# Performance work log

Hardware: AMD Instinct MI355X
Metric: run time of the kernel (lower is better)

The kernel has to match this reference:

```python
import jax, jax.numpy as jnp
import numpy as np

BN_EPS = 0.001

def conv2d(x, w, b, stride, pad):
    # x: NCHW, w: OIHW
    y = jax.lax.conv_general_dilated(x, w, (stride, stride), [(pad, pad), (pad, pad)],
                                     dimension_numbers=('NCHW', 'OIHW', 'NCHW'))
    return y + b[None, :, None, None]

def up2(x):
    return jnp.repeat(jnp.repeat(x, 2, axis=2), 2, axis=3)

def bn_eval(x, g, b):
    # BatchNorm in eval mode with fresh running stats (mean=0, var=1)
    inv = g / jnp.sqrt(1.0 + BN_EPS)
    return inv[None, :, None, None] * x + b[None, :, None, None]

def setup_inputs() -> dict:
    key = jax.random.key(0)
    ks = jax.random.split(key, 16)
    inp = {}
    inp['x_init'] = jax.random.uniform(ks[0], (8, 3, 1024, 1024), dtype=jnp.float32)
    inp['thresh'] = jax.random.uniform(ks[1], (2,), dtype=jnp.float32)
    inp['sample_w'] = jax.random.normal(ks[2], (3, 3, 4, 4), dtype=jnp.float32) * 0.1
    inp['sample_b'] = jax.random.normal(ks[3], (3,), dtype=jnp.float32) * 0.1
    inp['centers'] = jax.random.uniform(ks[4], (8,), dtype=jnp.float32)
    inp['pool1_w'] = jax.random.normal(ks[5], (3, 3, 2, 2), dtype=jnp.float32) * 0.2
    inp['pool1_b'] = jax.random.normal(ks[6], (3,), dtype=jnp.float32) * 0.1
    inp['pool2_w'] = jax.random.normal(ks[7], (3, 3, 2, 2), dtype=jnp.float32) * 0.2
    inp['pool2_b'] = jax.random.normal(ks[8], (3,), dtype=jnp.float32) * 0.1
    inp['ctx_conv_w'] = jax.random.normal(ks[9], (4, 3, 3, 3, 3), dtype=jnp.float32) * 0.2
    inp['ctx_conv_b'] = jax.random.normal(ks[10], (4, 3), dtype=jnp.float32) * 0.1
    inp['ctx_bn_g'] = jax.random.uniform(ks[11], (4, 3), dtype=jnp.float32) + 0.5
    inp['ctx_bn_b'] = jax.random.normal(ks[12], (4, 3), dtype=jnp.float32) * 0.1
    return inp

def _quant_idx_counts(t, mask, centers):
    # counts[k] = #(elements of t with mask and argmin center == k)
    idx = jnp.argmin((t[..., None] - centers) ** 2, axis=-1)  # same shape as t
    oh = idx[..., None] == jnp.arange(centers.shape[0])
    return jnp.sum((mask[..., None] & oh).astype(jnp.float32), axis=(0, 1, 2, 3))

def reference(x_init, thresh, sample_w, sample_b, centers,
              pool1_w, pool1_b, pool2_w, pool2_b,
              ctx_conv_w, ctx_conv_b, ctx_bn_g, ctx_bn_b):
    # spectral norm of sample conv weight (exact largest singular value)
    sigma = jnp.linalg.svd(sample_w.reshape(sample_w.shape[0], -1), compute_uv=False)[0]
    x = conv2d(x_init, sample_w / sigma, sample_b, 4, 0)  # [B,3,H/4,W/4]
    B, C, H, W = x.shape

    # ContextExtractor: conv_i(relu(bn_i(h))), stride 2 each
    h = x_init
    for i in range(3):
        h = conv2d(jax.nn.relu(bn_eval(h, ctx_bn_g[i], ctx_bn_b[i])), ctx_conv_w[i], ctx_conv_b[i], 2, 1)
    h1 = conv2d(jax.nn.relu(bn_eval(h, ctx_bn_g[3], ctx_bn_b[3])), ctx_conv_w[3], ctx_conv_b[3], 2, 1)
    feat_1 = (jnp.tanh(h) + 1.0) / 2.0    # [B,3,H/8,W/8]
    feat_2 = (jnp.tanh(h1) + 1.0) / 2.0   # [B,3,H/16,W/16]

    th_1, th_2 = thresh[0], thresh[1]
    feat_1_ = up2(feat_1)
    feat_2_ = up2(up2(feat_2))

    p1 = conv2d(x, pool1_w, pool1_b, 2, 0)    # half res
    p2 = conv2d(p1, pool2_w, pool2_b, 2, 0)   # quarter res
    ss_1 = up2(p1)
    ss_2 = up2(up2(p2))

    cond_2 = feat_2_ < th_2
    cond_1 = jnp.logical_and(jnp.logical_not(cond_2), feat_1_ < th_1)
    cond_0 = jnp.logical_not(jnp.logical_or(cond_1, cond_2))
    mask_1 = jnp.logical_and(up2(feat_2) >= th_2, feat_1 < th_1)  # half-res mask for p1
    mask_2 = feat_2 < th_2                                         # quarter-res mask for p2

    xq = jnp.where(cond_1, ss_1, x)
    xq = jnp.where(cond_2, ss_2, xq)

    # soft vector quantization against 8 learned centers
    d = (xq[..., None] - centers) ** 2                 # [B,C,H,W,8]
    soft = jnp.sum(centers * jax.nn.softmax(-d, axis=-1), axis=-1)

    # compression statistics (esti_cr; huffman real_cr omitted - host-side, non-tensor)
    esti_size = (jnp.sum(cond_0.astype(jnp.float32))
                 + jnp.sum(cond_1.astype(jnp.float32)) / 4.0
                 + jnp.sum(cond_2.astype(jnp.float32)) / 16.0)
    esti_cr = (1.0 / 16.0) * esti_size / (H * W * C * B)

    # histogram std over comp_data quantization indices, via masked counts
    counts = (_quant_idx_counts(x, cond_0, centers)
              + _quant_idx_counts(p1, mask_1, centers)
              + _quant_idx_counts(p2, mask_2, centers))
    counts = counts / jnp.sum(counts)
    std = jnp.std(counts, ddof=1)

    return (soft, esti_cr, std)
```

## Files before the change

kernel.cpp:

```cpp
#include <hip/hip_runtime.h>
#include <math.h>


#define SENT -1e30f
#define BSTR 72
#define BCH  (17 * BSTR)

__device__ __forceinline__ float featf(float h) { return 0.5f * (tanhf(h) + 1.0f); }

__device__ __forceinline__ void stage_raw(const float* __restrict__ base,
                                          float* __restrict__ L,
                                          int gr0, int gc0, int S, int t) {
    #pragma unroll
    for (int p = 0; p < 2; p++) {
        int idx = t + 256 * p;
        if (idx < 289) {
            int lr = idx / 17;
            int s  = idx - lr * 17;
            int gr = gr0 + lr;
            int gc = gc0 - 4 + 4 * s;
            float4 v;
            if (gr >= 0 && gr < S && gc >= 0)
                v = *(const float4*)(base + (size_t)gr * S + gc);
            else { v.x = SENT; v.y = SENT; v.z = SENT; v.w = SENT; }
            *(float4*)&L[lr * BSTR + 4 * s] = v;
        }
    }
}

__device__ __forceinline__ void stage_bn(const float* __restrict__ base,
                                         float* __restrict__ L,
                                         int gr0, int gc0, int S, int t,
                                         float inv, float bb) {
    #pragma unroll
    for (int p = 0; p < 2; p++) {
        int idx = t + 256 * p;
        if (idx < 289) {
            int lr = idx / 17;
            int s  = idx - lr * 17;
            int gr = gr0 + lr;
            int gc = gc0 - 4 + 4 * s;
            float4 v;
            if (gr >= 0 && gr < S && gc >= 0)
                v = *(const float4*)(base + (size_t)gr * S + gc);
            else { v.x = SENT; v.y = SENT; v.z = SENT; v.w = SENT; }
            v.x = fmaxf(fmaf(inv, v.x, bb), 0.0f);
            v.y = fmaxf(fmaf(inv, v.y, bb), 0.0f);
            v.z = fmaxf(fmaf(inv, v.z, bb), 0.0f);
            v.w = fmaxf(fmaf(inv, v.w, bb), 0.0f);
            *(float4*)&L[lr * BSTR + 4 * s] = v;
        }
    }
}

__global__ __launch_bounds__(256) void k_band_l0(
    const float* __restrict__ xin,
    const float* __restrict__ sw_g, const float* __restrict__ sb,
    const float* __restrict__ ctxw, const float* __restrict__ ctxb,
    const float* __restrict__ bng, const float* __restrict__ bnb,
    const float* __restrict__ p1w, const float* __restrict__ p1b,
    const float* __restrict__ p2w, const float* __restrict__ p2b,
    float* __restrict__ outX, float* __restrict__ outH0,
    float* __restrict__ outP1, float* __restrict__ outP2)
{
    __shared__ float sx[3 * BCH];

    int t = threadIdx.x, bid = blockIdx.x;
    int tileX = bid & 15, bandY = (bid >> 4) & 63, b = bid >> 10;

    int gr0 = bandY * 16 - 1;
    int gc0 = tileX * 64;
    #pragma unroll
    for (int c = 0; c < 3; c++)
        stage_raw(xin + ((size_t)(b * 3 + c) << 20), &sx[c * BCH], gr0, gc0, 1024, t);
    __syncthreads();

    {
        int ox = t & 31, oy = t >> 5;
        float v[3][9];
        const float* Lb = sx + (2 * oy) * BSTR + 2 * ox + 2;
        #pragma unroll
        for (int c = 0; c < 3; c++) {
            const float* Lc = Lb + c * BCH;
            #pragma unroll
            for (int kh = 0; kh < 3; kh++) {
                float2 u  = *(const float2*)(Lc + kh * BSTR);
                float2 w2 = *(const float2*)(Lc + kh * BSTR + 2);
                v[c][kh * 3 + 0] = u.y;
                v[c][kh * 3 + 1] = w2.x;
                v[c][kh * 3 + 2] = w2.y;
            }
        }
        #pragma unroll
        for (int c = 0; c < 3; c++) {
            float inv = bng[c] / sqrtf(1.001f), bb = bnb[c];
            #pragma unroll
            for (int k = 0; k < 9; k++)
                v[c][k] = fmaxf(fmaf(inv, v[c][k], bb), 0.0f);
        }
        float a0 = ctxb[0], a1 = ctxb[1], a2 = ctxb[2];
        #pragma unroll
        for (int c = 0; c < 3; c++)
            #pragma unroll
            for (int k = 0; k < 9; k++) {
                float tv = v[c][k];
                a0 = fmaf(ctxw[c * 9 + k],      tv, a0);
                a1 = fmaf(ctxw[27 + c * 9 + k], tv, a1);
                a2 = fmaf(ctxw[54 + c * 9 + k], tv, a2);
            }
        unsigned o = (unsigned)(b * 3) * 262144u
                   + (unsigned)(bandY * 8 + oy) * 512u + tileX * 32 + ox;
        outH0[o] = a0; outH0[o + 262144u] = a1; outH0[o + 524288u] = a2;
    }

    if (t < 64) {
        float p00 = 0.f, p01 = 0.f, p02 = 0.f, p11 = 0.f, p12 = 0.f, p22 = 0.f;
        if (t < 48) {
            float a0 = sw_g[t], a1 = sw_g[48 + t], a2 = sw_g[96 + t];
            p00 = a0 * a0; p01 = a0 * a1; p02 = a0 * a2;
            p11 = a1 * a1; p12 = a1 * a2; p22 = a2 * a2;
        }
        #pragma unroll
        for (int off = 32; off > 0; off >>= 1) {
            p00 += __shfl_down(p00, off); p01 += __shfl_down(p01, off);
            p02 += __shfl_down(p02, off); p11 += __shfl_down(p11, off);
            p12 += __shfl_down(p12, off); p22 += __shfl_down(p22, off);
        }
        float inv_sigma = 0.0f;
        if (t == 0) {
            float q = (p00 + p11 + p22) * (1.0f / 3.0f);
            float pp1 = p01 * p01 + p02 * p02 + p12 * p12;
            float pp2 = (p00 - q) * (p00 - q) + (p11 - q) * (p11 - q)
                      + (p22 - q) * (p22 - q) + 2.0f * pp1;
            float lam;
            if (pp2 < 1e-30f) lam = q;
            else {
                float pr = sqrtf(pp2 / 6.0f);
                float B00 = (p00 - q) / pr, B01 = p01 / pr, B02 = p02 / pr;
                float B11 = (p11 - q) / pr, B12 = p12 / pr, B22 = (p22 - q) / pr;
                float detB = B00 * (B11 * B22 - B12 * B12)
                           - B01 * (B01 * B22 - B12 * B02)
                           + B02 * (B01 * B12 - B11 * B02);
                float r = fminf(1.0f, fmaxf(-1.0f, 0.5f * detB));
                lam = q + 2.0f * pr * cosf(acosf(r) * (1.0f / 3.0f));
            }
            double G00 = p00, G01 = p01, G02 = p02, G11 = p11, G12 = p12, G22 = p22;
            double c2 = G00 + G11 + G22;
            double c1 = G00 * G11 - G01 * G01 + G00 * G22 - G02 * G02 + G11 * G22 - G12 * G12;
            double c0 = G00 * (G11 * G22 - G12 * G12) - G01 * (G01 * G22 - G12 * G02)
                      + G02 * (G01 * G12 - G11 * G02);
            double L = (double)lam;
            #pragma unroll
            for (int it = 0; it < 2; it++) {
                double pv = ((L - c2) * L + c1) * L - c0;
                double dv = (3.0 * L - 2.0 * c2) * L + c1;
                L -= pv / dv;
            }
            inv_sigma = (float)(1.0 / sqrt(L));
        }
        inv_sigma = __shfl(inv_sigma, 0);

        int xl = t & 15, yl = t >> 4;
        float4 r[3][4];
        #pragma unroll
        for (int c = 0; c < 3; c++)
            #pragma unroll
            for (int kh = 0; kh < 4; kh++)
                r[c][kh] = *(const float4*)&sx[c * BCH + (4 * yl + kh + 1) * BSTR + 4 * xl + 4];
        float s0 = 0.f, s1 = 0.f, s2 = 0.f;
        #pragma unroll
        for (int c = 0; c < 3; c++)
            #pragma unroll
            for (int kh = 0; kh < 4; kh++) {
                float4 vv = r[c][kh];
                const float* w0 = &sw_g[(0 * 3 + c) * 16 + kh * 4];
                const float* w1 = &sw_g[(1 * 3 + c) * 16 + kh * 4];
                const float* w2 = &sw_g[(2 * 3 + c) * 16 + kh * 4];
                s0 += w0[0] * vv.x + w0[1] * vv.y + w0[2] * vv.z + w0[3] * vv.w;
                s1 += w1[0] * vv.x + w1[1] * vv.y + w1[2] * vv.z + w1[3] * vv.w;
                s2 += w2[0] * vv.x + w2[1] * vv.y + w2[2] * vv.z + w2[3] * vv.w;
            }
        float x0 = fmaf(s0, inv_sigma, sb[0]);
        float x1 = fmaf(s1, inv_sigma, sb[1]);
        float x2 = fmaf(s2, inv_sigma, sb[2]);
        unsigned o = (unsigned)(b * 3) * 65536u
                   + (unsigned)(bandY * 4 + yl) * 256u + tileX * 16 + xl;
        outX[o] = x0; outX[o + 65536u] = x1; outX[o + 131072u] = x2;

        int sl = 2 * (t & 7) + 16 * (2 * ((t >> 3) & 1));
        float q0 = p1b[0], q1 = p1b[1], q2 = p1b[2];
        #pragma unroll
        for (int dy = 0; dy < 2; dy++)
            #pragma unroll
            for (int dx = 0; dx < 2; dx++) {
                int src = sl + dx + 16 * dy;
                float vx0 = __shfl(x0, src);
                float vx1 = __shfl(x1, src);
                float vx2 = __shfl(x2, src);
                int wi = dy * 2 + dx;
                q0 = fmaf(p1w[wi], vx0, q0); q0 = fmaf(p1w[4 + wi],  vx1, q0); q0 = fmaf(p1w[8 + wi],  vx2, q0);
                q1 = fmaf(p1w[12 + wi], vx0, q1); q1 = fmaf(p1w[16 + wi], vx1, q1); q1 = fmaf(p1w[20 + wi], vx2, q1);
                q2 = fmaf(p1w[24 + wi], vx0, q2); q2 = fmaf(p1w[28 + wi], vx1, q2); q2 = fmaf(p1w[32 + wi], vx2, q2);
            }
        if (t < 16) {
            int px = t & 7, py = t >> 3;
            unsigned op = (unsigned)(b * 3) * 16384u
                        + (unsigned)(bandY * 2 + py) * 128u + tileX * 8 + px;
            outP1[op] = q0; outP1[op + 16384u] = q1; outP1[op + 32768u] = q2;
        }

        int s2l = 2 * (t & 3);
        float r0 = p2b[0], r1 = p2b[1], r2 = p2b[2];
        #pragma unroll
        for (int dy = 0; dy < 2; dy++)
            #pragma unroll
            for (int dx = 0; dx < 2; dx++) {
                int src = s2l + dx + 8 * dy;
                float vq0 = __shfl(q0, src);
                float vq1 = __shfl(q1, src);
                float vq2 = __shfl(q2, src);
                int wi = dy * 2 + dx;
                r0 = fmaf(p2w[wi], vq0, r0); r0 = fmaf(p2w[4 + wi],  vq1, r0); r0 = fmaf(p2w[8 + wi],  vq2, r0);
                r1 = fmaf(p2w[12 + wi], vq0, r1); r1 = fmaf(p2w[16 + wi], vq1, r1); r1 = fmaf(p2w[20 + wi], vq2, r1);
                r2 = fmaf(p2w[24 + wi], vq0, r2); r2 = fmaf(p2w[28 + wi], vq1, r2); r2 = fmaf(p2w[32 + wi], vq2, r2);
            }
        if (t < 4) {
            unsigned op = (unsigned)(b * 3) * 4096u + (unsigned)bandY * 64u + tileX * 4 + t;
            outP2[op] = r0; outP2[op + 4096u] = r1; outP2[op + 8192u] = r2;
        }
    }
}

__global__ __launch_bounds__(256) void k_band_ctx(
    const float* __restrict__ in, float* __restrict__ outH, float* __restrict__ outF,
    const float* __restrict__ w, const float* __restrict__ bias,
    const float* __restrict__ bng, const float* __restrict__ bnb,
    int S, int tpxbits, int bandbits)
{
    __shared__ float sx[3 * BCH];
    int t = threadIdx.x, bid = blockIdx.x;
    int tileX = bid & ((1 << tpxbits) - 1);
    int bandY = (bid >> tpxbits) & ((1 << bandbits) - 1);
    int b = bid >> (tpxbits + bandbits);

    int gr0 = bandY * 16 - 1;
    int gc0 = tileX * 64;
    #pragma unroll
    for (int c = 0; c < 3; c++) {
        float inv = bng[c] / sqrtf(1.001f), bb = bnb[c];
        stage_bn(in + (size_t)(b * 3 + c) * S * S, &sx[c * BCH], gr0, gc0, S, t, inv, bb);
    }
    __syncthreads();

    int So = S >> 1;
    unsigned os = (unsigned)So * So;
    int ox = t & 31, oy = t >> 5;
    float v[3][9];
    const float* Lb = sx + (2 * oy) * BSTR + 2 * ox + 2;
    #pragma unroll
    for (int c = 0; c < 3; c++) {
        const float* Lc = Lb + c * BCH;
        #pragma unroll
        for (int kh = 0; kh < 3; kh++) {
            float2 u  = *(const float2*)(Lc + kh * BSTR);
            float2 w2 = *(const float2*)(Lc + kh * BSTR + 2);
            v[c][kh * 3 + 0] = u.y;
            v[c][kh * 3 + 1] = w2.x;
            v[c][kh * 3 + 2] = w2.y;
        }
    }
    float a0 = bias[0], a1 = bias[1], a2 = bias[2];
    #pragma unroll
    for (int c = 0; c < 3; c++)
        #pragma unroll
        for (int k = 0; k < 9; k++) {
            float tv = v[c][k];
            a0 = fmaf(w[c * 9 + k],      tv, a0);
            a1 = fmaf(w[27 + c * 9 + k], tv, a1);
            a2 = fmaf(w[54 + c * 9 + k], tv, a2);
        }
    unsigned o = (unsigned)(b * 3) * os + (unsigned)(bandY * 8 + oy) * So + tileX * 32 + ox;
    if (outH) { outH[o] = a0; outH[o + os] = a1; outH[o + 2 * os] = a2; }
    if (outF) { outF[o] = featf(a0); outF[o + os] = featf(a1); outF[o + 2 * os] = featf(a2); }
}

__device__ __forceinline__ int argmin8(float v, const float* __restrict__ sc) {
    float best = 1e30f; int ki = 0;
    #pragma unroll
    for (int k = 0; k < 8; k++) {
        float df = v - sc[k]; float dk = df * df;
        if (dk < best) { best = dk; ki = k; }
    }
    return ki;
}

__global__ __launch_bounds__(256) void k_final(
    const float* __restrict__ x, const float* __restrict__ f1,
    const float* __restrict__ f2, const float* __restrict__ p1,
    const float* __restrict__ p2, const float* __restrict__ thresh,
    const float* __restrict__ centers, float* __restrict__ out,
    int* __restrict__ partials)
{
    __shared__ int sh[4 * 12];
    int t = threadIdx.x;
    int lane = t & 63;
    int* shW = &sh[12 * (t >> 6)];
    if (lane < 12) shW[lane] = 0;
    float sc[8];
    #pragma unroll
    for (int k = 0; k < 8; k++) sc[k] = centers[k];
    __syncthreads();

    float th1 = thresh[0], th2 = thresh[1];
    int gid = blockIdx.x * 256 + t;
    int xc = gid & 255, y = (gid >> 8) & 255, b = gid >> 16;
    unsigned i2 = (unsigned)(((y >> 1) << 7) + (xc >> 1));
    unsigned i4 = (unsigned)(((y >> 2) << 6) + (xc >> 2));
    bool doM1 = ((y & 1) == 0) && ((xc & 1) == 0);
    bool doM2 = ((y & 3) == 0) && ((xc & 3) == 0);
    int c0n = 0, c1n = 0, c2n = 0;

    #pragma unroll
    for (int c = 0; c < 3; c++) {
        unsigned pc = (unsigned)(b * 3 + c);
        float f1v = f1[pc * 16384u + i2];
        float f2v = f2[pc * 4096u + i4];
        float p1v = p1[pc * 16384u + i2];
        float p2v = p2[pc * 4096u + i4];
        float xv  = x[pc * 65536u + (unsigned)((y << 8) + xc)];
        bool cond2 = f2v < th2;
        bool cond1 = (!cond2) && (f1v < th1);
        bool cond0 = !(cond1 || cond2);
        float xq = cond2 ? p2v : (cond1 ? p1v : xv);

        float d[8]; float dmin = 1e30f;
        #pragma unroll
        for (int k = 0; k < 8; k++) { float df = xq - sc[k]; d[k] = df * df; dmin = fminf(dmin, d[k]); }
        float se = 0.f, sn = 0.f;
        #pragma unroll
        for (int k = 0; k < 8; k++) { float e = __expf(dmin - d[k]); se += e; sn = fmaf(sc[k], e, sn); }
        out[pc * 65536u + (unsigned)((y << 8) + xc)] = sn / se;

        c0n += cond0; c1n += cond1; c2n += cond2;

        if (cond0) atomicAdd(&shW[argmin8(xv, sc)], 1);
        if (doM1 && (f2v >= th2) && (f1v < th1)) atomicAdd(&shW[argmin8(p1v, sc)], 1);
        if (doM2 && cond2) atomicAdd(&shW[argmin8(p2v, sc)], 1);
    }
    #pragma unroll
    for (int off = 32; off > 0; off >>= 1) {
        c0n += __shfl_down(c0n, off);
        c1n += __shfl_down(c1n, off);
        c2n += __shfl_down(c2n, off);
    }
    if (lane == 0) { atomicAdd(&shW[8], c0n); atomicAdd(&shW[9], c1n); atomicAdd(&shW[10], c2n); }
    __syncthreads();
    if (t < 12)
        partials[blockIdx.x * 12 + t] = sh[t] + sh[12 + t] + sh[24 + t] + sh[36 + t];
}

__global__ void k_reduce(const int* __restrict__ partials, float* __restrict__ out2) {
    __shared__ int accs[12];
    int t = threadIdx.x;
    if (t < 12) accs[t] = 0;
    __syncthreads();
    int s[12];
    #pragma unroll
    for (int k = 0; k < 12; k++) s[k] = 0;
    for (int r = t; r < 2048; r += 256) {
        const int* row = partials + r * 12;
        #pragma unroll
        for (int k = 0; k < 12; k++) s[k] += row[k];
    }
    #pragma unroll
    for (int k = 0; k < 12; k++) {
        #pragma unroll
        for (int off = 32; off > 0; off >>= 1) s[k] += __shfl_down(s[k], off);
    }
    if ((t & 63) == 0) {
        #pragma unroll
        for (int k = 0; k < 12; k++) if (s[k]) atomicAdd(&accs[k], s[k]);
    }
    __syncthreads();
    if (t == 0) {
        float cnt0 = (float)accs[8], cnt1 = (float)accs[9], cnt2 = (float)accs[10];
        float esti = cnt0 + cnt1 * 0.25f + cnt2 * 0.0625f;
        float cr = (1.0f / 16.0f) * esti / (256.0f * 256.0f * 3.0f * 8.0f);
        float cs[8]; float tot = 0.0f;
        #pragma unroll
        for (int k = 0; k < 8; k++) { cs[k] = (float)accs[k]; tot += cs[k]; }
        float mean = 0.0f;
        #pragma unroll
        for (int k = 0; k < 8; k++) { cs[k] /= tot; mean += cs[k]; }
        mean *= 0.125f;
        float var = 0.0f;
        #pragma unroll
        for (int k = 0; k < 8; k++) { float df = cs[k] - mean; var += df * df; }
        var *= (1.0f / 7.0f);
        out2[0] = cr;
        out2[1] = sqrtf(var);
    }
}

extern "C" void kernel_launch(void* const* d_in, const int* in_sizes, int n_in,
                              void* d_out, int out_size, void* d_ws, size_t ws_size,
                              hipStream_t stream) {
    const float* x_init   = (const float*)d_in[0];
    const float* thresh   = (const float*)d_in[1];
    const float* sample_w = (const float*)d_in[2];
    const float* sample_b = (const float*)d_in[3];
    const float* centers  = (const float*)d_in[4];
    const float* pool1_w  = (const float*)d_in[5];
    const float* pool1_b  = (const float*)d_in[6];
    const float* pool2_w  = (const float*)d_in[7];
    const float* pool2_b  = (const float*)d_in[8];
    const float* ctx_w    = (const float*)d_in[9];
    const float* ctx_b    = (const float*)d_in[10];
    const float* bn_g     = (const float*)d_in[11];
    const float* bn_b     = (const float*)d_in[12];
    float* out = (float*)d_out;

    float* wsf      = (float*)d_ws;
    int*   partials = (int*)wsf;
    float* bufX     = wsf + 32768;
    float* bufH0    = bufX  + 1572864;
    float* bufH1    = bufH0 + 6291456;
    float* bufH2    = bufH1 + 1572864;
    float* bufP1    = bufH2 + 393216;
    float* bufP2    = bufP1 + 393216;
    float* bufF1    = bufP2 + 98304;
    float* bufF2    = bufF1 + 393216;

    k_band_l0<<<8192, 256, 0, stream>>>(x_init, sample_w, sample_b,
                                        ctx_w, ctx_b, bn_g, bn_b,
                                        pool1_w, pool1_b, pool2_w, pool2_b,
                                        bufX, bufH0, bufP1, bufP2);
    k_band_ctx<<<2048, 256, 0, stream>>>(bufH0, bufH1, nullptr,
                                         ctx_w + 81,  ctx_b + 3, bn_g + 3, bn_b + 3,
                                         512, 3, 5);
    k_band_ctx<<<512, 256, 0, stream>>>(bufH1, bufH2, bufF1,
                                        ctx_w + 162, ctx_b + 6, bn_g + 6, bn_b + 6,
                                        256, 2, 4);
    k_band_ctx<<<128, 256, 0, stream>>>(bufH2, nullptr, bufF2,
                                        ctx_w + 243, ctx_b + 9, bn_g + 9, bn_b + 9,
                                        128, 1, 3);
    k_final<<<2048, 256, 0, stream>>>(bufX, bufF1, bufF2, bufP1, bufP2,
                                      thresh, centers, out, partials);
    k_reduce<<<1, 256, 0, stream>>>(partials, out + 1572864);
}
```

Measured before the change: 223.2 us.

## Fuse pairs of strided context conv layers via shared-memory halo recompute

Merges context conv layers 0 and 1 into the first kernel and layers 2 and 3 into a second kernel. Each block stages a larger halo tile, computes the intermediate layer into shared memory, and then applies the next conv. This removes the large H0 and H2 global round trips and two kernel launches. In exchange it adds redundant halo computation and more shared memory per block, and only 64 threads do the second-layer work.

```diff
diff --git a/kernel.cpp b/kernel.cpp
--- a/kernel.cpp
+++ b/kernel.cpp
@@ -3,120 +3,121 @@
 
 
 #define SENT -1e30f
-#define BSTR 72
-#define BCH  (17 * BSTR)
+#define SXSTR 72
+#define SXCH  (19 * SXSTR)
+#define H0STR 36
+#define H0CH  (9 * H0STR)
 
 __device__ __forceinline__ float featf(float h) { return 0.5f * (tanhf(h) + 1.0f); }
 
-__device__ __forceinline__ void stage_raw(const float* __restrict__ base,
-                                          float* __restrict__ L,
-                                          int gr0, int gc0, int S, int t) {
+__device__ __forceinline__ void stage19(const float* __restrict__ base,
+                                        float* __restrict__ L,
+                                        int gr0, int gc0, int S, int t) {
     #pragma unroll
     for (int p = 0; p < 2; p++) {
         int idx = t + 256 * p;
-        if (idx < 289) {
+        if (idx < 323) {
             int lr = idx / 17;
             int s  = idx - lr * 17;
             int gr = gr0 + lr;
-            int gc = gc0 - 4 + 4 * s;
+            int gc = gc0 + 4 * s;
             float4 v;
-            if (gr >= 0 && gr < S && gc >= 0)
+            if (gr >= 0 && gr < S && gc >= 0 && gc < S)
                 v = *(const float4*)(base + (size_t)gr * S + gc);
             else { v.x = SENT; v.y = SENT; v.z = SENT; v.w = SENT; }
-            *(float4*)&L[lr * BSTR + 4 * s] = v;
-        }
-    }
-}
-
-__device__ __forceinline__ void stage_bn(const float* __restrict__ base,
-                                         float* __restrict__ L,
-                                         int gr0, int gc0, int S, int t,
-                                         float inv, float bb) {
-    #pragma unroll
-    for (int p = 0; p < 2; p++) {
-        int idx = t + 256 * p;
-        if (idx < 289) {
-            int lr = idx / 17;
-            int s  = idx - lr * 17;
-            int gr = gr0 + lr;
-            int gc = gc0 - 4 + 4 * s;
-            float4 v;
-            if (gr >= 0 && gr < S && gc >= 0)
-                v = *(const float4*)(base + (size_t)gr * S + gc);
-            else { v.x = SENT; v.y = SENT; v.z = SENT; v.w = SENT; }
-            v.x = fmaxf(fmaf(inv, v.x, bb), 0.0f);
-            v.y = fmaxf(fmaf(inv, v.y, bb), 0.0f);
-            v.z = fmaxf(fmaf(inv, v.z, bb), 0.0f);
-            v.w = fmaxf(fmaf(inv, v.w, bb), 0.0f);
-            *(float4*)&L[lr * BSTR + 4 * s] = v;
-        }
-    }
-}
-
-__global__ __launch_bounds__(256) void k_band_l0(
+            *(float4*)&L[lr * SXSTR + 4 * s] = v;
+        }
+    }
+}
+
+__global__ __launch_bounds__(256) void k_fused01(
     const float* __restrict__ xin,
     const float* __restrict__ sw_g, const float* __restrict__ sb,
     const float* __restrict__ ctxw, const float* __restrict__ ctxb,
     const float* __restrict__ bng, const float* __restrict__ bnb,
     const float* __restrict__ p1w, const float* __restrict__ p1b,
     const float* __restrict__ p2w, const float* __restrict__ p2b,
-    float* __restrict__ outX, float* __restrict__ outH0,
+    float* __restrict__ outX, float* __restrict__ outH1,
     float* __restrict__ outP1, float* __restrict__ outP2)
 {
-    __shared__ float sx[3 * BCH];
+    __shared__ float sx[3 * SXCH];
+    __shared__ float sm[3 * H0CH];
 
     int t = threadIdx.x, bid = blockIdx.x;
     int tileX = bid & 15, bandY = (bid >> 4) & 63, b = bid >> 10;
 
-    int gr0 = bandY * 16 - 1;
-    int gc0 = tileX * 64;
+    int gr0 = bandY * 16 - 3;
+    int gc0 = tileX * 64 - 4;
     #pragma unroll
     for (int c = 0; c < 3; c++)
-        stage_raw(xin + ((size_t)(b * 3 + c) << 20), &sx[c * BCH], gr0, gc0, 1024, t);
+        stage19(xin + ((size_t)(b * 3 + c) << 20), &sx[c * SXCH], gr0, gc0, 1024, t);
     __syncthreads();
 
     {
-        int ox = t & 31, oy = t >> 5;
-        float v[3][9];
-        const float* Lb = sx + (2 * oy) * BSTR + 2 * ox + 2;
+        float inv0[3], bb0[3];
+        #pragma unroll
+        for (int c = 0; c < 3; c++) { inv0[c] = bng[c] / sqrtf(1.001f); bb0[c] = bnb[c]; }
+        #pragma unroll
+        for (int p = 0; p < 2; p++) {
+            int idx = t + 256 * p;
+            if (idx < 297) {
+                int lhy = idx / 33;
+                int lhx = idx - 33 * lhy;
+                bool oob = (bandY == 0 && lhy == 0) || (tileX == 0 && lhx == 0);
+                float a0 = ctxb[0], a1 = ctxb[1], a2 = ctxb[2];
+                #pragma unroll
+                for (int c = 0; c < 3; c++) {
+                    const float* basep = &sx[c * SXCH + 2 * lhy * SXSTR + 2 * lhx];
+                    float inv = inv0[c], bb = bb0[c];
+                    #pragma unroll
+                    for (int kh = 0; kh < 3; kh++) {
+                        float2 c0 = *(const float2*)(basep + kh * SXSTR);
+                        float2 c1 = *(const float2*)(basep + kh * SXSTR + 2);
+                        float t0 = fmaxf(fmaf(inv, c0.y, bb), 0.0f);
+                        float t1 = fmaxf(fmaf(inv, c1.x, bb), 0.0f);
+                        float t2 = fmaxf(fmaf(inv, c1.y, bb), 0.0f);
+                        int wi = c * 9 + kh * 3;
+                        a0 = fmaf(ctxw[wi], t0, a0); a0 = fmaf(ctxw[wi + 1], t1, a0); a0 = fmaf(ctxw[wi + 2], t2, a0);
+                        a1 = fmaf(ctxw[27 + wi], t0, a1); a1 = fmaf(ctxw[28 + wi], t1, a1); a1 = fmaf(ctxw[29 + wi], t2, a1);
+                        a2 = fmaf(ctxw[54 + wi], t0, a2); a2 = fmaf(ctxw[55 + wi], t1, a2); a2 = fmaf(ctxw[56 + wi], t2, a2);
+                    }
+                }
+                int o = lhy * H0STR + lhx;
+                if (oob) { a0 = SENT; a1 = SENT; a2 = SENT; }
+                sm[o] = a0; sm[H0CH + o] = a1; sm[2 * H0CH + o] = a2;
+            }
+        }
+    }
+    __syncthreads();
+
+    if (t < 64) {
+        int lx = t & 15, ly = t >> 4;
+        const float* w1c = ctxw + 81;
+        float a0 = ctxb[3], a1 = ctxb[4], a2 = ctxb[5];
         #pragma unroll
         for (int c = 0; c < 3; c++) {
-            const float* Lc = Lb + c * BCH;
+            float inv = bng[3 + c] / sqrtf(1.001f), bb = bnb[3 + c];
+            const float* mb = &sm[c * H0CH + 2 * ly * H0STR + 2 * lx];
             #pragma unroll
             for (int kh = 0; kh < 3; kh++) {
-                float2 u  = *(const float2*)(Lc + kh * BSTR);
-                float2 w2 = *(const float2*)(Lc + kh * BSTR + 2);
-                v[c][kh * 3 + 0] = u.y;
-                v[c][kh * 3 + 1] = w2.x;
-                v[c][kh * 3 + 2] = w2.y;
-            }
-        }
-        #pragma unroll
-        for (int c = 0; c < 3; c++) {
-            float inv = bng[c] / sqrtf(1.001f), bb = bnb[c];
-            #pragma unroll
-            for (int k = 0; k < 9; k++)
-                v[c][k] = fmaxf(fmaf(inv, v[c][k], bb), 0.0f);
-        }
-        float a0 = ctxb[0], a1 = ctxb[1], a2 = ctxb[2];
-        #pragma unroll
-        for (int c = 0; c < 3; c++)
-            #pragma unroll
-            for (int k = 0; k < 9; k++) {
-                float tv = v[c][k];
-                a0 = fmaf(ctxw[c * 9 + k],      tv, a0);
-                a1 = fmaf(ctxw[27 + c * 9 + k], tv, a1);
-                a2 = fmaf(ctxw[54 + c * 9 + k], tv, a2);
-            }
-        unsigned o = (unsigned)(b * 3) * 262144u
-                   + (unsigned)(bandY * 8 + oy) * 512u + tileX * 32 + ox;
-        outH0[o] = a0; outH0[o + 262144u] = a1; outH0[o + 524288u] = a2;
-    }
-
-    if (t < 64) {
+                float2 c0 = *(const float2*)(mb + kh * H0STR);
+                float c2v = mb[kh * H0STR + 2];
+                float t0 = fmaxf(fmaf(inv, c0.x, bb), 0.0f);
+                float t1 = fmaxf(fmaf(inv, c0.y, bb), 0.0f);
+                float t2 = fmaxf(fmaf(inv, c2v, bb), 0.0f);
+                int wi = c * 9 + kh * 3;
+                a0 = fmaf(w1c[wi], t0, a0); a0 = fmaf(w1c[wi + 1], t1, a0); a0 = fmaf(w1c[wi + 2], t2, a0);
+                a1 = fmaf(w1c[27 + wi], t0, a1); a1 = fmaf(w1c[28 + wi], t1, a1); a1 = fmaf(w1c[29 + wi], t2, a1);
+                a2 = fmaf(w1c[54 + wi], t0, a2); a2 = fmaf(w1c[55 + wi], t1, a2); a2 = fmaf(w1c[56 + wi], t2, a2);
+            }
+        }
+        unsigned o = (unsigned)(b * 3) * 65536u + (unsigned)(bandY * 4 + ly) * 256u + tileX * 16 + lx;
+        outH1[o] = a0; outH1[o + 65536u] = a1; outH1[o + 131072u] = a2;
+    } else if (t < 128) {
+        int tl = t - 64;
         float p00 = 0.f, p01 = 0.f, p02 = 0.f, p11 = 0.f, p12 = 0.f, p22 = 0.f;
-        if (t < 48) {
-            float a0 = sw_g[t], a1 = sw_g[48 + t], a2 = sw_g[96 + t];
+        if (tl < 48) {
+            float a0 = sw_g[tl], a1 = sw_g[48 + tl], a2 = sw_g[96 + tl];
             p00 = a0 * a0; p01 = a0 * a1; p02 = a0 * a2;
             p11 = a1 * a1; p12 = a1 * a2; p22 = a2 * a2;
         }
@@ -127,7 +128,7 @@
             p12 += __shfl_down(p12, off); p22 += __shfl_down(p22, off);
         }
         float inv_sigma = 0.0f;
-        if (t == 0) {
+        if (tl == 0) {
             float q = (p00 + p11 + p22) * (1.0f / 3.0f);
             float pp1 = p01 * p01 + p02 * p02 + p12 * p12;
             float pp2 = (p00 - q) * (p00 - q) + (p11 - q) * (p11 - q)
@@ -160,13 +161,13 @@
         }
         inv_sigma = __shfl(inv_sigma, 0);
 
-        int xl = t & 15, yl = t >> 4;
+        int xl = tl & 15, yl = tl >> 4;
         float4 r[3][4];
         #pragma unroll
         for (int c = 0; c < 3; c++)
             #pragma unroll
             for (int kh = 0; kh < 4; kh++)
-                r[c][kh] = *(const float4*)&sx[c * BCH + (4 * yl + kh + 1) * BSTR + 4 * xl + 4];
+                r[c][kh] = *(const float4*)&sx[c * SXCH + (4 * yl + 3 + kh) * SXSTR + 4 * xl + 4];
         float s0 = 0.f, s1 = 0.f, s2 = 0.f;
         #pragma unroll
         for (int c = 0; c < 3; c++)
@@ -183,11 +184,10 @@
         float x0 = fmaf(s0, inv_sigma, sb[0]);
         float x1 = fmaf(s1, inv_sigma, sb[1]);
         float x2 = fmaf(s2, inv_sigma, sb[2]);
-        unsigned o = (unsigned)(b * 3) * 65536u
-                   + (unsigned)(bandY * 4 + yl) * 256u + tileX * 16 + xl;
+        unsigned o = (unsigned)(b * 3) * 65536u + (unsigned)(bandY * 4 + yl) * 256u + tileX * 16 + xl;
         outX[o] = x0; outX[o + 65536u] = x1; outX[o + 131072u] = x2;
 
-        int sl = 2 * (t & 7) + 16 * (2 * ((t >> 3) & 1));
+        int sl = 2 * (tl & 7) + 32 * ((tl >> 3) & 1);
         float q0 = p1b[0], q1 = p1b[1], q2 = p1b[2];
         #pragma unroll
         for (int dy = 0; dy < 2; dy++)
@@ -202,14 +202,13 @@
                 q1 = fmaf(p1w[12 + wi], vx0, q1); q1 = fmaf(p1w[16 + wi], vx1, q1); q1 = fmaf(p1w[20 + wi], vx2, q1);
                 q2 = fmaf(p1w[24 + wi], vx0, q2); q2 = fmaf(p1w[28 + wi], vx1, q2); q2 = fmaf(p1w[32 + wi], vx2, q2);
             }
-        if (t < 16) {
-            int px = t & 7, py = t >> 3;
-            unsigned op = (unsigned)(b * 3) * 16384u
-                        + (unsigned)(bandY * 2 + py) * 128u + tileX * 8 + px;
+        if (tl < 16) {
+            int px = tl & 7, py = tl >> 3;
+            unsigned op = (unsigned)(b * 3) * 16384u + (unsigned)(bandY * 2 + py) * 128u + tileX * 8 + px;
             outP1[op] = q0; outP1[op + 16384u] = q1; outP1[op + 32768u] = q2;
         }
 
-        int s2l = 2 * (t & 3);
+        int s2l = 2 * (tl & 3);
         float r0 = p2b[0], r1 = p2b[1], r2 = p2b[2];
         #pragma unroll
         for (int dy = 0; dy < 2; dy++)
@@ -224,64 +223,98 @@
                 r1 = fmaf(p2w[12 + wi], vq0, r1); r1 = fmaf(p2w[16 + wi], vq1, r1); r1 = fmaf(p2w[20 + wi], vq2, r1);
                 r2 = fmaf(p2w[24 + wi], vq0, r2); r2 = fmaf(p2w[28 + wi], vq1, r2); r2 = fmaf(p2w[32 + wi], vq2, r2);
             }
-        if (t < 4) {
-            unsigned op = (unsigned)(b * 3) * 4096u + (unsigned)bandY * 64u + tileX * 4 + t;
+        if (tl < 4) {
+            unsigned op = (unsigned)(b * 3) * 4096u + (unsigned)bandY * 64u + tileX * 4 + tl;
             outP2[op] = r0; outP2[op + 4096u] = r1; outP2[op + 8192u] = r2;
         }
     }
 }
 
-__global__ __launch_bounds__(256) void k_band_ctx(
-    const float* __restrict__ in, float* __restrict__ outH, float* __restrict__ outF,
-    const float* __restrict__ w, const float* __restrict__ bias,
-    const float* __restrict__ bng, const float* __restrict__ bnb,
-    int S, int tpxbits, int bandbits)
+__global__ __launch_bounds__(256) void k_fused23(
+    const float* __restrict__ h1, float* __restrict__ outF1, float* __restrict__ outF2,
+    const float* __restrict__ ctxw, const float* __restrict__ ctxb,
+    const float* __restrict__ bng, const float* __restrict__ bnb)
 {
-    __shared__ float sx[3 * BCH];
+    __shared__ float sx[3 * SXCH];
+    __shared__ float sm[3 * H0CH];
+
     int t = threadIdx.x, bid = blockIdx.x;
-    int tileX = bid & ((1 << tpxbits) - 1);
-    int bandY = (bid >> tpxbits) & ((1 << bandbits) - 1);
-    int b = bid >> (tpxbits + bandbits);
-
-    int gr0 = bandY * 16 - 1;
-    int gc0 = tileX * 64;
-    #pragma unroll
-    for (int c = 0; c < 3; c++) {
-        float inv = bng[c] / sqrtf(1.001f), bb = bnb[c];
-        stage_bn(in + (size_t)(b * 3 + c) * S * S, &sx[c * BCH], gr0, gc0, S, t, inv, bb);
-    }
-    __syncthreads();
-
-    int So = S >> 1;
-    unsigned os = (unsigned)So * So;
-    int ox = t & 31, oy = t >> 5;
-    float v[3][9];
-    const float* Lb = sx + (2 * oy) * BSTR + 2 * ox + 2;
-    #pragma unroll
-    for (int c = 0; c < 3; c++) {
-        const float* Lc = Lb + c * BCH;
-        #pragma unroll
-        for (int kh = 0; kh < 3; kh++) {
-            float2 u  = *(const float2*)(Lc + kh * BSTR);
-            float2 w2 = *(const float2*)(Lc + kh * BSTR + 2);
-            v[c][kh * 3 + 0] = u.y;
-            v[c][kh * 3 + 1] = w2.x;
-            v[c][kh * 3 + 2] = w2.y;
-        }
-    }
-    float a0 = bias[0], a1 = bias[1], a2 = bias[2];
+    int tileX = bid & 3, bandY = (bid >> 2) & 15, b = bid >> 6;
+
+    int gr0 = bandY * 16 - 3;
+    int gc0 = tileX * 64 - 4;
     #pragma unroll
     for (int c = 0; c < 3; c++)
-        #pragma unroll
-        for (int k = 0; k < 9; k++) {
-            float tv = v[c][k];
-            a0 = fmaf(w[c * 9 + k],      tv, a0);
-            a1 = fmaf(w[27 + c * 9 + k], tv, a1);
-            a2 = fmaf(w[54 + c * 9 + k], tv, a2);
-        }
-    unsigned o = (unsigned)(b * 3) * os + (unsigned)(bandY * 8 + oy) * So + tileX * 32 + ox;
-    if (outH) { outH[o] = a0; outH[o + os] = a1; outH[o + 2 * os] = a2; }
-    if (outF) { outF[o] = featf(a0); outF[o + os] = featf(a1); outF[o + 2 * os] = featf(a2); }
+        stage19(h1 + (size_t)(b * 3 + c) * 65536, &sx[c * SXCH], gr0, gc0, 256, t);
+    __syncthreads();
+
+    {
+        const float* w2c = ctxw + 162;
+        float inv2[3], bb2[3];
+        #pragma unroll
+        for (int c = 0; c < 3; c++) { inv2[c] = bng[6 + c] / sqrtf(1.001f); bb2[c] = bnb[6 + c]; }
+        #pragma unroll
+        for (int p = 0; p < 2; p++) {
+            int idx = t + 256 * p;
+            if (idx < 297) {
+                int lhy = idx / 33;
+                int lhx = idx - 33 * lhy;
+                bool oob = (bandY == 0 && lhy == 0) || (tileX == 0 && lhx == 0);
+                float a0 = ctxb[6], a1 = ctxb[7], a2 = ctxb[8];
+                #pragma unroll
+                for (int c = 0; c < 3; c++) {
+                    const float* basep = &sx[c * SXCH + 2 * lhy * SXSTR + 2 * lhx];
+                    float inv = inv2[c], bb = bb2[c];
+                    #pragma unroll
+                    for (int kh = 0; kh < 3; kh++) {
+                        float2 c0 = *(const float2*)(basep + kh * SXSTR);
+                        float2 c1 = *(const float2*)(basep + kh * SXSTR + 2);
+                        float t0 = fmaxf(fmaf(inv, c0.y, bb), 0.0f);
+                        float t1 = fmaxf(fmaf(inv, c1.x, bb), 0.0f);
+                        float t2 = fmaxf(fmaf(inv, c1.y, bb), 0.0f);
+                        int wi = c * 9 + kh * 3;
+                        a0 = fmaf(w2c[wi], t0, a0); a0 = fmaf(w2c[wi + 1], t1, a0); a0 = fmaf(w2c[wi + 2], t2, a0);
+                        a1 = fmaf(w2c[27 + wi], t0, a1); a1 = fmaf(w2c[28 + wi], t1, a1); a1 = fmaf(w2c[29 + wi], t2, a1);
+                        a2 = fmaf(w2c[54 + wi], t0, a2); a2 = fmaf(w2c[55 + wi], t1, a2); a2 = fmaf(w2c[56 + wi], t2, a2);
+                    }
+                }
+                int o = lhy * H0STR + lhx;
+                if (!oob && lhy >= 1 && lhx >= 1) {
+                    unsigned fo = (unsigned)(b * 3) * 16384u
+                                + (unsigned)(8 * bandY + lhy - 1) * 128u + 32 * tileX + lhx - 1;
+                    outF1[fo] = featf(a0); outF1[fo + 16384u] = featf(a1); outF1[fo + 32768u] = featf(a2);
+                }
+                if (oob) { a0 = SENT; a1 = SENT; a2 = SENT; }
+                sm[o] = a0; sm[H0CH + o] = a1; sm[2 * H0CH + o] = a2;
+            }
+        }
+    }
+    __syncthreads();
+
+    if (t < 64) {
+        int lx = t & 15, ly = t >> 4;
+        const float* w3c = ctxw + 243;
+        float a0 = ctxb[9], a1 = ctxb[10], a2 = ctxb[11];
+        #pragma unroll
+        for (int c = 0; c < 3; c++) {
+            float inv = bng[9 + c] / sqrtf(1.001f), bb = bnb[9 + c];
+            const float* mb = &sm[c * H0CH + 2 * ly * H0STR + 2 * lx];
+            #pragma unroll
+            for (int kh = 0; kh < 3; kh++) {
+                float2 c0 = *(const float2*)(mb + kh * H0STR);
+                float c2v = mb[kh * H0STR + 2];
+                float t0 = fmaxf(fmaf(inv, c0.x, bb), 0.0f);
+                float t1 = fmaxf(fmaf(inv, c0.y, bb), 0.0f);
+                float t2 = fmaxf(fmaf(inv, c2v, bb), 0.0f);
+                int wi = c * 9 + kh * 3;
+                a0 = fmaf(w3c[wi], t0, a0); a0 = fmaf(w3c[wi + 1], t1, a0); a0 = fmaf(w3c[wi + 2], t2, a0);
+                a1 = fmaf(w3c[27 + wi], t0, a1); a1 = fmaf(w3c[28 + wi], t1, a1); a1 = fmaf(w3c[29 + wi], t2, a1);
+                a2 = fmaf(w3c[54 + wi], t0, a2); a2 = fmaf(w3c[55 + wi], t1, a2); a2 = fmaf(w3c[56 + wi], t2, a2);
+            }
+        }
+        unsigned o = (unsigned)(b * 3) * 4096u + (unsigned)(bandY * 4 + ly) * 64u + tileX * 16 + lx;
+        outF2[o] = featf(a0); outF2[o + 4096u] = featf(a1); outF2[o + 8192u] = featf(a2);
+    }
 }
 
 __device__ __forceinline__ int argmin8(float v, const float* __restrict__ sc) {
@@ -423,27 +456,18 @@
     float* wsf      = (float*)d_ws;
     int*   partials = (int*)wsf;
     float* bufX     = wsf + 32768;
-    float* bufH0    = bufX  + 1572864;
-    float* bufH1    = bufH0 + 6291456;
-    float* bufH2    = bufH1 + 1572864;
-    float* bufP1    = bufH2 + 393216;
+    float* bufH1    = bufX  + 1572864;
+    float* bufP1    = bufH1 + 1572864;
     float* bufP2    = bufP1 + 393216;
     float* bufF1    = bufP2 + 98304;
     float* bufF2    = bufF1 + 393216;
 
-    k_band_l0<<<8192, 256, 0, stream>>>(x_init, sample_w, sample_b,
+    k_fused01<<<8192, 256, 0, stream>>>(x_init, sample_w, sample_b,
                                         ctx_w, ctx_b, bn_g, bn_b,
                                         pool1_w, pool1_b, pool2_w, pool2_b,
-                                        bufX, bufH0, bufP1, bufP2);
-    k_band_ctx<<<2048, 256, 0, stream>>>(bufH0, bufH1, nullptr,
-                                         ctx_w + 81,  ctx_b + 3, bn_g + 3, bn_b + 3,
-                                         512, 3, 5);
-    k_band_ctx<<<512, 256, 0, stream>>>(bufH1, bufH2, bufF1,
-                                        ctx_w + 162, ctx_b + 6, bn_g + 6, bn_b + 6,
-                                        256, 2, 4);
-    k_band_ctx<<<128, 256, 0, stream>>>(bufH2, nullptr, bufF2,
-                                        ctx_w + 243, ctx_b + 9, bn_g + 9, bn_b + 9,
-                                        128, 1, 3);
+                                        bufX, bufH1, bufP1, bufP2);
+    k_fused23<<<512, 256, 0, stream>>>(bufH1, bufF1, bufF2,
+                                       ctx_w, ctx_b, bn_g, bn_b);
     k_final<<<2048, 256, 0, stream>>>(bufX, bufF1, bufF2, bufP1, bufP2,
                                       thresh, centers, out, partials);
     k_reduce<<<1, 256, 0, stream>>>(partials, out + 1572864);
```

Measured after the change: 213.0 us. 1.05x faster.
